# Kernel optimization log

Hardware: AMD Instinct MI355X
Metric: run time of the kernel (lower is better)

The kernel has to match this reference:

```python
import jax, jax.numpy as jnp
import numpy as np

B, N, C, H, D = 1, 256, 128, 4, 32  # batch, n_res, c_z, heads, head_dim
LN_EPS = 1e-5


def setup_inputs() -> dict:
    key = jax.random.key(0)
    ks = jax.random.split(key, 10)
    s = 0.02
    return {
        "act": jax.random.normal(ks[0], (B, N, N, C), dtype=jnp.float32),
        "mask": jnp.ones((B, N, N), dtype=jnp.float32),
        "ln_g": jnp.ones((C,), dtype=jnp.float32),
        "ln_b": jnp.zeros((C,), dtype=jnp.float32),
        "w2d": jax.random.normal(ks[1], (C, H), dtype=jnp.float32) * s,
        "wq": jax.random.normal(ks[2], (C, H, D), dtype=jnp.float32) * s,
        "wk": jax.random.normal(ks[3], (C, H, D), dtype=jnp.float32) * s,
        "wv": jax.random.normal(ks[4], (C, H, D), dtype=jnp.float32) * s,
        "wg": jax.random.normal(ks[5], (C, H, D), dtype=jnp.float32) * s,
        "bg": jnp.ones((H, D), dtype=jnp.float32),
        "wo": jax.random.normal(ks[6], (H, D, C), dtype=jnp.float32) * s,
        "bo": jnp.zeros((C,), dtype=jnp.float32),
    }


def reference(act, mask, ln_g, ln_b, w2d, wq, wk, wv, wg, bg, wo, bo):
    # LayerNorm over channel dim
    mu = jnp.mean(act, axis=-1, keepdims=True)
    var = jnp.mean(jnp.square(act - mu), axis=-1, keepdims=True)
    x = (act - mu) * jax.lax.rsqrt(var + LN_EPS) * ln_g + ln_b  # [B,N,N,C]

    # mask bias: [B, I, 1, 1, K]
    mask_bias = (1e9 * (mask - 1.0))[:, :, None, None, :]
    # nonbatched pair bias: [B, 1, H, Q, K]
    nb_bias = jnp.einsum('bqkc,ch->bhqk', x, w2d)[:, None]

    scale = 1.0 / jnp.sqrt(jnp.asarray(D, dtype=x.dtype))
    q = jnp.einsum('bijc,chd->bijhd', x, wq) * scale  # [B,I,Q,H,D]
    k = jnp.einsum('bijc,chd->bijhd', x, wk)
    v = jnp.einsum('bijc,chd->bijhd', x, wv)

    logits = jnp.einsum('biqhd,bikhd->bihqk', q, k) + mask_bias + nb_bias
    a = jax.nn.softmax(logits, axis=-1)  # [B,I,H,Q,K]
    o = jnp.einsum('bihqk,bikhd->biqhd', a, v)  # [B,I,Q,H,D]

    g = jax.nn.sigmoid(jnp.einsum('bijc,chd->bijhd', x, wg) + bg)
    o = o * g
    out = jnp.einsum('biqhd,hdc->biqc', o, wo) + bo  # [B,N,N,C]
    return out
```

## Files before the change

kernel.cpp:

```cpp
#include <hip/hip_runtime.h>

#define QK_SCALE 0.17677669529663689f

typedef float f4 __attribute__((ext_vector_type(4)));
typedef short bf16x8 __attribute__((ext_vector_type(8)));
typedef float f32x4 __attribute__((ext_vector_type(4)));
typedef unsigned short us4 __attribute__((ext_vector_type(4)));

__device__ __forceinline__ unsigned short f2bf(float x){
  unsigned int u = __float_as_uint(x);
  u += 0x7fffu + ((u >> 16) & 1u);
  return (unsigned short)(u >> 16);
}
__device__ __forceinline__ float bf2f(unsigned short h){
  return __uint_as_float(((unsigned int)h) << 16);
}
__device__ __forceinline__ f32x4 mfma16(bf16x8 a, bf16x8 b, f32x4 c){
  return __builtin_amdgcn_mfma_f32_16x16x32_bf16(a, b, c, 0, 0, 0);
}
__device__ __forceinline__ void gload_lds16(const void* g, void* s){
  __builtin_amdgcn_global_load_lds(
      (const __attribute__((address_space(1))) unsigned int*)g,
      (__attribute__((address_space(3))) unsigned int*)s, 16, 0, 0);
}

__global__ __launch_bounds__(256)
void k_prep(const float* __restrict__ wq, const float* __restrict__ wk,
            const float* __restrict__ wv, const float* __restrict__ wg,
            const float* __restrict__ wo, unsigned short* __restrict__ pk)
{
  const int m = blockIdx.x;
  const float* W = (m==0)? wq : (m==1)? wk : (m==2)? wv : (m==3)? wg : wo;
  const float scale = (m==0)? QK_SCALE : 1.0f;
  unsigned short* dst = pk + (long)m * 32768;
  for (int ent = threadIdx.x; ent < 2048; ent += 256){
    const int l = ent & 63, ktn = ent >> 6;
    const int kt = ktn & 3, nt = ktn >> 2;
    unsigned short* ph = dst + ((nt*4 + kt)*2 + 0)*512 + l*8;
    unsigned short* pl = dst + ((nt*4 + kt)*2 + 1)*512 + l*8;
    #pragma unroll
    for (int e = 0; e < 8; ++e){
      const int row = kt*32 + (l>>4)*8 + e;
      const int col = nt*16 + (l&15);
      float v = W[row*128 + col] * scale;
      unsigned short hh = f2bf(v);
      ph[e] = hh;
      pl[e] = f2bf(v - bf2f(hh));
    }
  }
}

__global__ __launch_bounds__(512, 4)
void k_proj(const float* __restrict__ act, const float* __restrict__ ln_g,
            const float* __restrict__ ln_b, const float* __restrict__ w2d,
            const unsigned short* __restrict__ pk, const float* __restrict__ bg,
            unsigned short* __restrict__ qf, unsigned short* __restrict__ kf,
            unsigned short* __restrict__ vt, unsigned short* __restrict__ gg,
            float* __restrict__ b2d)
{
  __shared__ unsigned short afr[8*4*2*512];
  __shared__ unsigned short sc[4*640];
  const int t = threadIdx.x, w = t>>6, l = t&63, g16 = l>>4, c = l&15;
  const long p0 = (long)blockIdx.x * 128;
  const int bi = (int)(p0 >> 8);
  const int qb0 = (int)(p0 & 255);
  const int row = w*16 + c;

  {
    const float* ap = act + (p0 + row)*128;
    f4 xv[4][2];
    #pragma unroll
    for (int kt = 0; kt < 4; ++kt){
      xv[kt][0] = *(const f4*)(ap + kt*32 + g16*8);
      xv[kt][1] = *(const f4*)(ap + kt*32 + g16*8 + 4);
    }
    float s = 0.f, s2 = 0.f;
    #pragma unroll
    for (int kt = 0; kt < 4; ++kt)
      #pragma unroll
      for (int u = 0; u < 2; ++u)
        #pragma unroll
        for (int e = 0; e < 4; ++e){
          float x = xv[kt][u][e]; s += x; s2 += x*x;
        }
    s += __shfl_xor(s,16); s2 += __shfl_xor(s2,16);
    s += __shfl_xor(s,32); s2 += __shfl_xor(s2,32);
    const float mu = s*(1.f/128.f);
    const float iv = rsqrtf(fmaxf(s2*(1.f/128.f)-mu*mu,0.f)+1e-5f);

    float pb0=0.f, pb1=0.f, pb2=0.f, pb3=0.f;
    #pragma unroll
    for (int kt = 0; kt < 4; ++kt){
      bf16x8 hv, lv;
      #pragma unroll
      for (int u = 0; u < 2; ++u){
        const int cb = kt*32 + g16*8 + u*4;
        f4 lg = *(const f4*)(ln_g + cb);
        f4 lb = *(const f4*)(ln_b + cb);
        #pragma unroll
        for (int e0 = 0; e0 < 4; ++e0){
          float vv = (xv[kt][u][e0]-mu)*iv*lg[e0] + lb[e0];
          f4 wp = *(const f4*)(w2d + (cb+e0)*4);
          pb0 += vv*wp[0]; pb1 += vv*wp[1]; pb2 += vv*wp[2]; pb3 += vv*wp[3];
          unsigned short hh = f2bf(vv);
          hv[u*4+e0] = (short)hh;
          lv[u*4+e0] = (short)f2bf(vv - bf2f(hh));
        }
      }
      *(bf16x8*)&afr[((w*4+kt)*2+0)*512 + l*8] = hv;
      *(bf16x8*)&afr[((w*4+kt)*2+1)*512 + l*8] = lv;
    }
    pb0 += __shfl_xor(pb0,16); pb1 += __shfl_xor(pb1,16);
    pb2 += __shfl_xor(pb2,16); pb3 += __shfl_xor(pb3,16);
    pb0 += __shfl_xor(pb0,32); pb1 += __shfl_xor(pb1,32);
    pb2 += __shfl_xor(pb2,32); pb3 += __shfl_xor(pb3,32);
    const float pbsel = (g16==0)? pb0 : (g16==1)? pb1 : (g16==2)? pb2 : pb3;
    b2d[g16*65536 + (int)p0 + row] = pbsel;
  }
  __syncthreads();

  #pragma unroll
  for (int pass = 0; pass < 2; ++pass){
    bf16x8 bh0[4], bl0[4], bh1[4], bl1[4];
    { const int ntg = w*4 + pass*2;
      #pragma unroll
      for (int kt = 0; kt < 4; ++kt){
        bh0[kt] = *(const bf16x8*)(pk + ((ntg*4+kt)*2+0)*512 + l*8);
        bl0[kt] = *(const bf16x8*)(pk + ((ntg*4+kt)*2+1)*512 + l*8);
        bh1[kt] = *(const bf16x8*)(pk + (((ntg+1)*4+kt)*2+0)*512 + l*8);
        bl1[kt] = *(const bf16x8*)(pk + (((ntg+1)*4+kt)*2+1)*512 + l*8);
      } }
    for (int rt = 0; rt < 8; ++rt){
      bf16x8 ah[4], al[4];
      #pragma unroll
      for (int kt = 0; kt < 4; ++kt){
        ah[kt] = *(const bf16x8*)&afr[((rt*4+kt)*2+0)*512 + l*8];
        al[kt] = *(const bf16x8*)&afr[((rt*4+kt)*2+1)*512 + l*8];
      }
      f32x4 a0 = {0.f,0.f,0.f,0.f}, a1 = {0.f,0.f,0.f,0.f};
      #pragma unroll
      for (int kt = 0; kt < 4; ++kt){
        a0 = mfma16(ah[kt], bh0[kt], a0);
        a1 = mfma16(ah[kt], bh1[kt], a1);
        a0 = mfma16(ah[kt], bl0[kt], a0);
        a1 = mfma16(ah[kt], bl1[kt], a1);
        a0 = mfma16(al[kt], bh0[kt], a0);
        a1 = mfma16(al[kt], bh1[kt], a1);
      }
      if (w < 4){
        unsigned short* scw = sc + w*640;
        #pragma unroll
        for (int j = 0; j < 4; ++j){
          scw[(g16*4+j)*40 + c]      = f2bf(a0[j]);
          scw[(g16*4+j)*40 + 16 + c] = f2bf(a1[j]);
        }
        asm volatile("" ::: "memory");
        bf16x8 fr = *(const bf16x8*)&scw[c*40 + g16*8];
        const int head = (w&1)*2 + pass;
        unsigned short* dst = (w < 2) ? qf : kf;
        *(bf16x8*)&dst[(((long)bi*4+head)*16 + (qb0>>4) + rt)*512 + l*8] = fr;
        asm volatile("" ::: "memory");
      } else if (w < 6){
        const int ntv0 = (w-4)*4 + pass*2;
        const int kv = qb0 + rt*16 + g16*4;
        #pragma unroll
        for (int np = 0; np < 2; ++np){
          const int colg = (ntv0+np)*16 + c;
          const int head = colg >> 5, d = colg & 31;
          f32x4 aa = np ? a1 : a0;
          us4 v4;
          #pragma unroll
          for (int j = 0; j < 4; ++j) v4[j] = f2bf(aa[j]);
          const int vb = (d*512 + kv*2) ^ ((d&7)<<4);
          *(us4*)((char*)vt + ((long)bi*4+head)*16384 + vb) = v4;
        }
      } else {
        const int colb = (w-6)*64 + pass*32;
        const int row0 = (int)p0 + rt*16 + g16*4;
        const float bg0 = bg[colb + c];
        const float bg1 = bg[colb + 16 + c];
        #pragma unroll
        for (int j = 0; j < 4; ++j){
          float g0 = 1.f/(1.f + __expf(-(a0[j] + bg0)));
          float g1 = 1.f/(1.f + __expf(-(a1[j] + bg1)));
          gg[(row0+j)*128 + colb + c]      = f2bf(g0);
          gg[(row0+j)*128 + colb + 16 + c] = f2bf(g1);
        }
      }
    }
  }
}

__global__ __launch_bounds__(256, 3)
void k_attn(const unsigned short* __restrict__ qf, const unsigned short* __restrict__ kfg,
            const unsigned short* __restrict__ vt, const unsigned short* __restrict__ gg,
            const float* __restrict__ b2d, const float* __restrict__ mask,
            unsigned short* __restrict__ obf)
{
  __shared__ unsigned short k_s[16*512];
  __shared__ unsigned short v_s[8192];
  __shared__ unsigned short p_s[4*2048];
  __shared__ float mb_s[256];
  const int t = threadIdx.x, w = t>>6, l = t&63, g16 = l>>4, c = l&15;
  const int bi = blockIdx.x >> 2, h = blockIdx.x & 3;
  const int base = (bi*4+h)*8192;

  #pragma unroll
  for (int cc = 0; cc < 8; ++cc){
    const int ch = w*8 + cc;
    if (ch < 16) gload_lds16(kfg + base + ch*512 + l*8, k_s + ch*512);
    else         gload_lds16(vt + base + (ch-16)*512 + l*8, v_s + (ch-16)*512);
  }
  mb_s[t] = 1e9f * (mask[bi*256 + t] - 1.0f);
  asm volatile("s_waitcnt vmcnt(0)" ::: "memory");
  __syncthreads();

  char* pw = (char*)(p_s + w*2048);
  const int swz = (c&7)<<4;

  for (int im = 0; im < 4; ++im){
    const int q0 = w*64 + im*16;
    const bf16x8 qfr = *(const bf16x8*)(qf + base + (q0>>4)*512 + l*8);
    const float* bq = b2d + h*65536 + (q0 + c)*256 + g16*4;
    f32x4 sa[16];
    #pragma unroll
    for (int nt = 0; nt < 16; ++nt){
      f4 bv = *(const f4*)(bq + nt*16);
      f4 mv = *(const f4*)&mb_s[nt*16 + g16*4];
      f32x4 ci;
      ci[0]=bv[0]+mv[0]; ci[1]=bv[1]+mv[1]; ci[2]=bv[2]+mv[2]; ci[3]=bv[3]+mv[3];
      sa[nt] = mfma16(*(const bf16x8*)(k_s + nt*512 + l*8), qfr, ci);
    }
    float mx = fmaxf(fmaxf(sa[0][0], sa[0][1]), fmaxf(sa[0][2], sa[0][3]));
    #pragma unroll
    for (int nt = 1; nt < 16; ++nt)
      mx = fmaxf(mx, fmaxf(fmaxf(sa[nt][0], sa[nt][1]), fmaxf(sa[nt][2], sa[nt][3])));
    mx = fmaxf(mx, __shfl_xor(mx, 16));
    mx = fmaxf(mx, __shfl_xor(mx, 32));
    const float nmx = -mx * 1.44269504f;
    float sum = 0.f;
    #pragma unroll
    for (int nt = 0; nt < 16; ++nt){
      #pragma unroll
      for (int j = 0; j < 4; ++j){
        float e = exp2f(fmaf(sa[nt][j], 1.44269504f, nmx));
        sa[nt][j] = e; sum += e;
      }
    }
    sum += __shfl_xor(sum, 16);
    sum += __shfl_xor(sum, 32);
    const float inv = 1.f / sum;
    f32x4 oa0 = {0.f,0.f,0.f,0.f}, oa1 = {0.f,0.f,0.f,0.f};
    #pragma unroll
    for (int ph2 = 0; ph2 < 2; ++ph2){
      #pragma unroll
      for (int ntl = 0; ntl < 8; ++ntl){
        const int nt = ph2*8 + ntl;
        us4 pk4;
        pk4[0] = f2bf(sa[nt][0]); pk4[1] = f2bf(sa[nt][1]);
        pk4[2] = f2bf(sa[nt][2]); pk4[3] = f2bf(sa[nt][3]);
        *(us4*)(pw + c*256 + ((ntl*32 + g16*8) ^ swz)) = pk4;
      }
      asm volatile("s_waitcnt lgkmcnt(0)" ::: "memory");
      __builtin_amdgcn_sched_barrier(0);
      #pragma unroll
      for (int ktl = 0; ktl < 4; ++ktl){
        const int kt = ph2*4 + ktl;
        bf16x8 pf = *(const bf16x8*)(pw + c*256 + ((ktl*64 + g16*16) ^ swz));
        const int vb0 = ((c*512      + kt*64 + g16*16) ^ swz);
        const int vb1 = (((16+c)*512 + kt*64 + g16*16) ^ swz);
        oa0 = mfma16(*(const bf16x8*)((const char*)v_s + vb0), pf, oa0);
        oa1 = mfma16(*(const bf16x8*)((const char*)v_s + vb1), pf, oa1);
      }
      asm volatile("" ::: "memory");
      __builtin_amdgcn_sched_barrier(0);
    }
    const int row = bi*256 + q0 + c;
    us4 gv0 = *(const us4*)&gg[row*128 + h*32 + g16*4];
    us4 gv1 = *(const us4*)&gg[row*128 + h*32 + 16 + g16*4];
    us4 o0, o1;
    #pragma unroll
    for (int j = 0; j < 4; ++j){
      o0[j] = f2bf(oa0[j] * inv * bf2f(gv0[j]));
      o1[j] = f2bf(oa1[j] * inv * bf2f(gv1[j]));
    }
    *(us4*)&obf[row*128 + h*32 + g16*4]      = o0;
    *(us4*)&obf[row*128 + h*32 + 16 + g16*4] = o1;
  }
}

__global__ __launch_bounds__(512, 4)
void k_out(const unsigned short* __restrict__ obf, const unsigned short* __restrict__ pko,
           const float* __restrict__ bo, float* __restrict__ out)
{
  __shared__ unsigned short afr[32*512];
  const int t = threadIdx.x, w = t>>6, l = t&63, g16 = l>>4, c = l&15;
  const long p0 = (long)blockIdx.x * 128;

  #pragma unroll
  for (int u = 0; u < 4; ++u){
    const int pr = w*4 + u;
    const int rt = pr >> 2, kt = pr & 3;
    gload_lds16(obf + (p0 + rt*16 + c)*128 + kt*32 + g16*8, afr + pr*512);
  }
  asm volatile("s_waitcnt vmcnt(0)" ::: "memory");
  __syncthreads();

  bf16x8 bh[4], bl[4];
  #pragma unroll
  for (int kt = 0; kt < 4; ++kt){
    bh[kt] = *(const bf16x8*)(pko + ((w*4+kt)*2+0)*512 + l*8);
    bl[kt] = *(const bf16x8*)(pko + ((w*4+kt)*2+1)*512 + l*8);
  }
  const float bov = bo[w*16 + c];
  for (int rt = 0; rt < 8; ++rt){
    f32x4 a0 = {bov, bov, bov, bov};
    #pragma unroll
    for (int kt = 0; kt < 4; ++kt){
      bf16x8 af = *(const bf16x8*)&afr[(rt*4+kt)*512 + l*8];
      a0 = mfma16(af, bh[kt], a0);
      a0 = mfma16(af, bl[kt], a0);
    }
    const int row0 = (int)p0 + rt*16 + g16*4;
    #pragma unroll
    for (int j = 0; j < 4; ++j)
      out[(row0+j)*128 + w*16 + c] = a0[j];
  }
}

extern "C" void kernel_launch(void* const* d_in, const int* in_sizes, int n_in,
                              void* d_out, int out_size, void* d_ws, size_t ws_size,
                              hipStream_t stream) {
  const float* act  = (const float*)d_in[0];
  const float* mask = (const float*)d_in[1];
  const float* ln_g = (const float*)d_in[2];
  const float* ln_b = (const float*)d_in[3];
  const float* w2d  = (const float*)d_in[4];
  const float* wq   = (const float*)d_in[5];
  const float* wk   = (const float*)d_in[6];
  const float* wv   = (const float*)d_in[7];
  const float* wg   = (const float*)d_in[8];
  const float* bg   = (const float*)d_in[9];
  const float* wo   = (const float*)d_in[10];
  const float* bo   = (const float*)d_in[11];
  float* out = (float*)d_out;

  char* ws = (char*)d_ws;
  unsigned short* qf  = (unsigned short*)(ws);
  unsigned short* kfb = (unsigned short*)(ws + 16777216L);
  unsigned short* vt  = (unsigned short*)(ws + 33554432L);
  unsigned short* gg  = (unsigned short*)(ws + 50331648L);
  unsigned short* obf = (unsigned short*)(ws + 67108864L);
  float* b2d = (float*)(ws + 83886080L);
  unsigned short* pk = (unsigned short*)(ws + 84934656L);

  k_prep<<<5, 256, 0, stream>>>(wq, wk, wv, wg, wo, pk);
  k_proj<<<512, 512, 0, stream>>>(act, ln_g, ln_b, w2d, pk, bg,
                                  qf, kfb, vt, gg, b2d);
  k_attn<<<1024, 256, 0, stream>>>(qf, kfb, vt, gg, b2d, mask, obf);
  k_out<<<512, 512, 0, stream>>>(obf, pk + 4*32768, bo, out);
}
```

Measured before the change: 110.1 us.

## Use 8 waves per attention block and hardware packed bf16 conversion

The attention kernel now runs 512 threads per block, so each wave handles 32 query rows instead of 64. The per-wave P staging buffer is halved and the softmax-times-V loop runs in four phases instead of two. Float-to-bf16 rounding now uses the v_cvt_pk_bf16_f32 instruction, which packs two values at once and replaces the manual integer rounding. The aim is more waves in flight to hide latency and fewer ALU instructions, at the cost of higher register pressure under the new launch bounds and more phase syncs per wave.

Result: no change. 110.9 us (+0.8%).

```diff
diff --git a/kernel.cpp b/kernel.cpp
--- a/kernel.cpp
+++ b/kernel.cpp
@@ -6,6 +6,7 @@
 typedef short bf16x8 __attribute__((ext_vector_type(8)));
 typedef float f32x4 __attribute__((ext_vector_type(4)));
 typedef unsigned short us4 __attribute__((ext_vector_type(4)));
+typedef unsigned int u32x2 __attribute__((ext_vector_type(2)));
 
 __device__ __forceinline__ unsigned short f2bf(float x){
   unsigned int u = __float_as_uint(x);
@@ -14,6 +15,11 @@
 }
 __device__ __forceinline__ float bf2f(unsigned short h){
   return __uint_as_float(((unsigned int)h) << 16);
+}
+__device__ __forceinline__ unsigned int cvtpk(float lo, float hi){
+  unsigned int r;
+  asm volatile("v_cvt_pk_bf16_f32 %0, %1, %2" : "=v"(r) : "v"(lo), "v"(hi));
+  return r;
 }
 __device__ __forceinline__ f32x4 mfma16(bf16x8 a, bf16x8 b, f32x4 c){
   return __builtin_amdgcn_mfma_f32_16x16x32_bf16(a, b, c, 0, 0, 0);
@@ -191,7 +197,7 @@
   }
 }
 
-__global__ __launch_bounds__(256, 3)
+__global__ __launch_bounds__(512, 4)
 void k_attn(const unsigned short* __restrict__ qf, const unsigned short* __restrict__ kfg,
             const unsigned short* __restrict__ vt, const unsigned short* __restrict__ gg,
             const float* __restrict__ b2d, const float* __restrict__ mask,
@@ -199,27 +205,27 @@
 {
   __shared__ unsigned short k_s[16*512];
   __shared__ unsigned short v_s[8192];
-  __shared__ unsigned short p_s[4*2048];
+  __shared__ unsigned short p_s[8*1024];
   __shared__ float mb_s[256];
   const int t = threadIdx.x, w = t>>6, l = t&63, g16 = l>>4, c = l&15;
   const int bi = blockIdx.x >> 2, h = blockIdx.x & 3;
   const int base = (bi*4+h)*8192;
 
   #pragma unroll
-  for (int cc = 0; cc < 8; ++cc){
-    const int ch = w*8 + cc;
+  for (int cc = 0; cc < 4; ++cc){
+    const int ch = w*4 + cc;
     if (ch < 16) gload_lds16(kfg + base + ch*512 + l*8, k_s + ch*512);
     else         gload_lds16(vt + base + (ch-16)*512 + l*8, v_s + (ch-16)*512);
   }
-  mb_s[t] = 1e9f * (mask[bi*256 + t] - 1.0f);
+  if (t < 256) mb_s[t] = 1e9f * (mask[bi*256 + t] - 1.0f);
   asm volatile("s_waitcnt vmcnt(0)" ::: "memory");
   __syncthreads();
 
-  char* pw = (char*)(p_s + w*2048);
+  char* pw = (char*)(p_s + w*1024);
   const int swz = (c&7)<<4;
 
-  for (int im = 0; im < 4; ++im){
-    const int q0 = w*64 + im*16;
+  for (int im = 0; im < 2; ++im){
+    const int q0 = w*32 + im*16;
     const bf16x8 qfr = *(const bf16x8*)(qf + base + (q0>>4)*512 + l*8);
     const float* bq = b2d + h*65536 + (q0 + c)*256 + g16*4;
     f32x4 sa[16];
@@ -252,21 +258,21 @@
     const float inv = 1.f / sum;
     f32x4 oa0 = {0.f,0.f,0.f,0.f}, oa1 = {0.f,0.f,0.f,0.f};
     #pragma unroll
-    for (int ph2 = 0; ph2 < 2; ++ph2){
-      #pragma unroll
-      for (int ntl = 0; ntl < 8; ++ntl){
-        const int nt = ph2*8 + ntl;
-        us4 pk4;
-        pk4[0] = f2bf(sa[nt][0]); pk4[1] = f2bf(sa[nt][1]);
-        pk4[2] = f2bf(sa[nt][2]); pk4[3] = f2bf(sa[nt][3]);
-        *(us4*)(pw + c*256 + ((ntl*32 + g16*8) ^ swz)) = pk4;
+    for (int p4 = 0; p4 < 4; ++p4){
+      #pragma unroll
+      for (int ntl = 0; ntl < 4; ++ntl){
+        const int nt = p4*4 + ntl;
+        u32x2 pk2;
+        pk2[0] = cvtpk(sa[nt][0], sa[nt][1]);
+        pk2[1] = cvtpk(sa[nt][2], sa[nt][3]);
+        *(u32x2*)(pw + c*128 + ((ntl*32 + g16*8) ^ swz)) = pk2;
       }
       asm volatile("s_waitcnt lgkmcnt(0)" ::: "memory");
       __builtin_amdgcn_sched_barrier(0);
       #pragma unroll
-      for (int ktl = 0; ktl < 4; ++ktl){
-        const int kt = ph2*4 + ktl;
-        bf16x8 pf = *(const bf16x8*)(pw + c*256 + ((ktl*64 + g16*16) ^ swz));
+      for (int ktl = 0; ktl < 2; ++ktl){
+        const int kt = p4*2 + ktl;
+        bf16x8 pf = *(const bf16x8*)(pw + c*128 + ((ktl*64 + g16*16) ^ swz));
         const int vb0 = ((c*512      + kt*64 + g16*16) ^ swz);
         const int vb1 = (((16+c)*512 + kt*64 + g16*16) ^ swz);
         oa0 = mfma16(*(const bf16x8*)((const char*)v_s + vb0), pf, oa0);
@@ -278,14 +284,13 @@
     const int row = bi*256 + q0 + c;
     us4 gv0 = *(const us4*)&gg[row*128 + h*32 + g16*4];
     us4 gv1 = *(const us4*)&gg[row*128 + h*32 + 16 + g16*4];
-    us4 o0, o1;
-    #pragma unroll
-    for (int j = 0; j < 4; ++j){
-      o0[j] = f2bf(oa0[j] * inv * bf2f(gv0[j]));
-      o1[j] = f2bf(oa1[j] * inv * bf2f(gv1[j]));
-    }
-    *(us4*)&obf[row*128 + h*32 + g16*4]      = o0;
-    *(us4*)&obf[row*128 + h*32 + 16 + g16*4] = o1;
+    u32x2 o0, o1;
+    o0[0] = cvtpk(oa0[0]*inv*bf2f(gv0[0]), oa0[1]*inv*bf2f(gv0[1]));
+    o0[1] = cvtpk(oa0[2]*inv*bf2f(gv0[2]), oa0[3]*inv*bf2f(gv0[3]));
+    o1[0] = cvtpk(oa1[0]*inv*bf2f(gv1[0]), oa1[1]*inv*bf2f(gv1[1]));
+    o1[1] = cvtpk(oa1[2]*inv*bf2f(gv1[2]), oa1[3]*inv*bf2f(gv1[3]));
+    *(u32x2*)&obf[row*128 + h*32 + g16*4]      = o0;
+    *(u32x2*)&obf[row*128 + h*32 + 16 + g16*4] = o1;
   }
 }
 
@@ -357,6 +362,6 @@
   k_prep<<<5, 256, 0, stream>>>(wq, wk, wv, wg, wo, pk);
   k_proj<<<512, 512, 0, stream>>>(act, ln_g, ln_b, w2d, pk, bg,
                                   qf, kfb, vt, gg, b2d);
-  k_attn<<<1024, 256, 0, stream>>>(qf, kfb, vt, gg, b2d, mask, obf);
+  k_attn<<<1024, 512, 0, stream>>>(qf, kfb, vt, gg, b2d, mask, obf);
   k_out<<<512, 512, 0, stream>>>(obf, pk + 4*32768, bo, out);
 }
```
